# Performance work log

Measured on AMD Instinct MI355X. Metric: run time of the kernel, lower is better.

## Reference

```python
import jax, jax.numpy as jnp
import numpy as np
import math

B, S, D, H = 2, 2048, 2048, 16
DH = D // H  # 128


def _rope(x, cos, sin):
    # x: [b, s, h, dh]; cos/sin: [s, dh//2]
    b, s, h, dh = x.shape
    x2 = x.reshape(b, s, h, dh // 2, 2)
    a, bb = x2[..., 0], x2[..., 1]
    c = cos[None, :, None, :]
    sn = sin[None, :, None, :]
    out = jnp.stack([a * c - bb * sn, a * sn + bb * c], axis=-1)
    return out.reshape(b, s, h, dh)


def setup_inputs() -> dict:
    key = jax.random.key(0)
    ks = jax.random.split(key, 6)
    x = jax.random.normal(ks[0], (B, S, D), dtype=jnp.float32)
    # RoPE frequencies (theta=10000) as cos/sin of shape [S, DH//2]
    inv_freq = 1.0 / (10000.0 ** (np.arange(0, DH, 2, dtype=np.float32) / DH))
    t = np.arange(S, dtype=np.float32)
    ang = jnp.asarray(np.outer(t, inv_freq))  # [S, DH//2]
    freqs_cos = jnp.cos(ang)
    freqs_sin = jnp.sin(ang)
    # causal additive mask [1,1,S,S]
    neg = jnp.finfo(jnp.float32).min
    mask = jnp.where(jnp.tril(jnp.ones((S, S), dtype=bool)), 0.0, neg)[None, None]
    sc = 0.02
    wq = jax.random.normal(ks[1], (D, D), dtype=jnp.float32) * sc
    wk = jax.random.normal(ks[2], (D, D), dtype=jnp.float32) * sc
    wv = jax.random.normal(ks[3], (D, D), dtype=jnp.float32) * sc
    wo = jax.random.normal(ks[4], (D, D), dtype=jnp.float32) * sc
    return {"x": x, "freqs_cos": freqs_cos, "freqs_sin": freqs_sin,
            "mask": mask, "wq": wq, "wk": wk, "wv": wv, "wo": wo}


def reference(x, freqs_cos, freqs_sin, mask, wq, wk, wv, wo):
    b, s, _ = x.shape
    # torch Linear: y = x @ W.T (weights stored [out, in])
    xq = (x @ wq.T).reshape(b, s, H, DH)
    xk = (x @ wk.T).reshape(b, s, H, DH)
    xv = (x @ wv.T).reshape(b, s, H, DH)
    xq = _rope(xq, freqs_cos, freqs_sin)
    xk = _rope(xk, freqs_cos, freqs_sin)
    # [b, h, s, dh]
    q = xq.transpose(0, 2, 1, 3)
    k = xk.transpose(0, 2, 1, 3)
    v = xv.transpose(0, 2, 1, 3)
    scores = jnp.einsum('bhqd,bhkd->bhqk', q, k) / math.sqrt(DH)
    scores = scores + mask
    attn = jax.nn.softmax(scores, axis=-1)  # dropout p=0 (eval)
    out = jnp.einsum('bhqk,bhkd->bhqd', attn, v)
    out = out.transpose(0, 2, 1, 3).reshape(b, s, D)
    return out @ wo.T
```

## Files before the change

kernel.cpp:

```cpp
#include <hip/hip_runtime.h>

#define B_ 2
#define S_ 2048
#define D_ 2048
#define H_ 16
#define DH_ 128

typedef __bf16 bf16_8 __attribute__((ext_vector_type(8)));
typedef __bf16 bf16_4 __attribute__((ext_vector_type(4)));
typedef float f32x4 __attribute__((ext_vector_type(4)));

__device__ __forceinline__ f32x4 mfma16(bf16_8 a, bf16_8 b, f32x4 c) {
  return __builtin_amdgcn_mfma_f32_16x16x32_bf16(a, b, c, 0, 0, 0);
}

__device__ __forceinline__ bf16_8 load8(const float* p) {
  f32x4 a = *(const f32x4*)p;
  f32x4 b = *(const f32x4*)(p + 4);
  bf16_8 r;
  r[0] = (__bf16)a[0]; r[1] = (__bf16)a[1]; r[2] = (__bf16)a[2]; r[3] = (__bf16)a[3];
  r[4] = (__bf16)b[0]; r[5] = (__bf16)b[1]; r[6] = (__bf16)b[2]; r[7] = (__bf16)b[3];
  return r;
}

__device__ __forceinline__ void async16(const __bf16* g, __bf16* l) {
  __builtin_amdgcn_global_load_lds(
      (const __attribute__((address_space(1))) void*)g,
      (__attribute__((address_space(3))) void*)l, 16, 0, 0);
}

__global__ __launch_bounds__(256) void cvt_all(
    const float* __restrict__ x, const float* __restrict__ wq,
    const float* __restrict__ wk, const float* __restrict__ wv,
    const float* __restrict__ wo, __bf16* __restrict__ xb,
    __bf16* __restrict__ wqb, __bf16* __restrict__ wkb,
    __bf16* __restrict__ wvb, __bf16* __restrict__ wob)
{
  const int W8 = (D_ * D_) / 8;
  int i = blockIdx.x * 256 + threadIdx.x;
  if (i < 2 * W8) {
    *(bf16_8*)(xb + (size_t)i * 8) = load8(x + (size_t)i * 8);
  } else {
    int j = i - 2 * W8;
    int sel = j >> 19, off = j & (W8 - 1);
    const float* s = sel == 0 ? wq : sel == 1 ? wk : sel == 2 ? wv : wo;
    __bf16* d = sel == 0 ? wqb : sel == 1 ? wkb : sel == 2 ? wvb : wob;
    *(bf16_8*)(d + (size_t)off * 8) = load8(s + (size_t)off * 8);
  }
}

template <bool WB>
__global__ __launch_bounds__(256) void qkv_gemm(
    const __bf16* __restrict__ A,
    const float* __restrict__ wqf, const float* __restrict__ wkf,
    const float* __restrict__ wvf,
    const __bf16* __restrict__ wqb, const __bf16* __restrict__ wkb,
    const __bf16* __restrict__ wvb,
    const float* __restrict__ fc, const float* __restrict__ fs,
    __bf16* __restrict__ Qo, __bf16* __restrict__ Ko, __bf16* __restrict__ Vo)
{
  __shared__ __bf16 As[128][32];
  __shared__ __bf16 Ws[128][WB ? 32 : 40];
  const int tid = threadIdx.x;
  const int wave = tid >> 6, lane = tid & 63;
  const int quad = lane >> 4, l16 = lane & 15;
  const int m0 = blockIdx.y * 128, n0 = blockIdx.x * 128;
  const int wsel = n0 >> 11, nloc = n0 & 2047;
  const int wm = (wave >> 1) * 64, wn = (wave & 1) * 64;
  const __bf16* agl = A + (size_t)(m0 + wave * 32 + (lane >> 2)) * 2048 + (lane & 3) * 8;
  f32x4 acc[4][4] = {};
  if (WB) {
    const __bf16* Wb = wsel == 0 ? wqb : wsel == 1 ? wkb : wvb;
    const __bf16* wgl = Wb + (size_t)(nloc + wave * 32 + (lane >> 2)) * 2048 + (lane & 3) * 8;
    for (int k0 = 0; k0 < 2048; k0 += 32) {
      __syncthreads();
      async16(agl + k0,             &As[wave * 32][0]);
      async16(agl + 16 * 2048 + k0, &As[wave * 32 + 16][0]);
      async16(wgl + k0,             &Ws[wave * 32][0]);
      async16(wgl + 16 * 2048 + k0, &Ws[wave * 32 + 16][0]);
      __syncthreads();
      bf16_8 af[4], bfr[4];
      for (int i = 0; i < 4; ++i) {
        af[i]  = *(const bf16_8*)&As[wm + i * 16 + l16][quad * 8];
        bfr[i] = *(const bf16_8*)&Ws[wn + i * 16 + l16][quad * 8];
      }
      for (int mi = 0; mi < 4; ++mi)
        for (int ni = 0; ni < 4; ++ni)
          acc[mi][ni] = mfma16(af[mi], bfr[ni], acc[mi][ni]);
    }
  } else {
    const float* W = wsel == 0 ? wqf : wsel == 1 ? wkf : wvf;
    const int srow = tid >> 1, scol = (tid & 1) * 16;
    const float* wg = W + (size_t)(nloc + srow) * 2048 + scol;
    for (int k0 = 0; k0 < 2048; k0 += 32) {
      __syncthreads();
      async16(agl + k0,             &As[wave * 32][0]);
      async16(agl + 16 * 2048 + k0, &As[wave * 32 + 16][0]);
      *(bf16_8*)&Ws[srow][scol]     = load8(wg + k0);
      *(bf16_8*)&Ws[srow][scol + 8] = load8(wg + k0 + 8);
      __syncthreads();
      bf16_8 af[4], bfr[4];
      for (int i = 0; i < 4; ++i) {
        af[i]  = *(const bf16_8*)&As[wm + i * 16 + l16][quad * 8];
        bfr[i] = *(const bf16_8*)&Ws[wn + i * 16 + l16][quad * 8];
      }
      for (int mi = 0; mi < 4; ++mi)
        for (int ni = 0; ni < 4; ++ni)
          acc[mi][ni] = mfma16(af[mi], bfr[ni], acc[mi][ni]);
    }
  }
  if (wsel < 2) {
    const float qscale = wsel == 0 ? 0.08838834764831845f * 1.4426950408889634f
                                   : 1.0f;
    __bf16* O = wsel == 0 ? Qo : Ko;
    for (int mi = 0; mi < 4; ++mi)
      for (int ni = 0; ni < 4; ++ni)
        for (int r = 0; r < 4; ++r) {
          int row = m0 + wm + mi * 16 + quad * 4 + r;
          int col = nloc + wn + ni * 16 + l16;
          float self = acc[mi][ni][r];
          float oth = __shfl_xor(self, 1);
          int s = row & (S_ - 1);
          int dh = col & (DH_ - 1);
          float c = fc[s * (DH_ / 2) + (dh >> 1)];
          float sn = fs[s * (DH_ / 2) + (dh >> 1)];
          float o = (dh & 1) ? (oth * sn + self * c) : (self * c - oth * sn);
          O[(size_t)row * 2048 + col] = (__bf16)(o * qscale);
        }
  } else {
    for (int mi = 0; mi < 4; ++mi)
      for (int ni = 0; ni < 4; ++ni) {
        int col = nloc + wn + ni * 16 + l16;
        int row0 = m0 + wm + mi * 16 + quad * 4;
        int b = row0 >> 11, s = row0 & (S_ - 1);
        int h = col >> 7, dh = col & (DH_ - 1);
        bf16_4 pk;
        for (int r = 0; r < 4; ++r) pk[r] = (__bf16)acc[mi][ni][r];
        *(bf16_4*)(Vo + ((size_t)(b * H_ + h) * DH_ + dh) * S_ + s) = pk;
      }
  }
}

template <bool WB>
__global__ __launch_bounds__(256) void out_gemm(
    const __bf16* __restrict__ A, const float* __restrict__ Wf,
    const __bf16* __restrict__ Wb, float* __restrict__ C)
{
  __shared__ __bf16 As[128][32];
  __shared__ __bf16 Ws[128][WB ? 32 : 40];
  const int tid = threadIdx.x;
  const int wave = tid >> 6, lane = tid & 63;
  const int quad = lane >> 4, l16 = lane & 15;
  const int m0 = blockIdx.y * 128, n0 = blockIdx.x * 128;
  const int wm = (wave >> 1) * 64, wn = (wave & 1) * 64;
  const __bf16* agl = A + (size_t)(m0 + wave * 32 + (lane >> 2)) * 2048 + (lane & 3) * 8;
  f32x4 acc[4][4] = {};
  if (WB) {
    const __bf16* wgl = Wb + (size_t)(n0 + wave * 32 + (lane >> 2)) * 2048 + (lane & 3) * 8;
    for (int k0 = 0; k0 < 2048; k0 += 32) {
      __syncthreads();
      async16(agl + k0,             &As[wave * 32][0]);
      async16(agl + 16 * 2048 + k0, &As[wave * 32 + 16][0]);
      async16(wgl + k0,             &Ws[wave * 32][0]);
      async16(wgl + 16 * 2048 + k0, &Ws[wave * 32 + 16][0]);
      __syncthreads();
      bf16_8 af[4], bfr[4];
      for (int i = 0; i < 4; ++i) {
        af[i]  = *(const bf16_8*)&As[wm + i * 16 + l16][quad * 8];
        bfr[i] = *(const bf16_8*)&Ws[wn + i * 16 + l16][quad * 8];
      }
      for (int mi = 0; mi < 4; ++mi)
        for (int ni = 0; ni < 4; ++ni)
          acc[mi][ni] = mfma16(af[mi], bfr[ni], acc[mi][ni]);
    }
  } else {
    const int srow = tid >> 1, scol = (tid & 1) * 16;
    const float* wg = Wf + (size_t)(n0 + srow) * 2048 + scol;
    for (int k0 = 0; k0 < 2048; k0 += 32) {
      __syncthreads();
      async16(agl + k0,             &As[wave * 32][0]);
      async16(agl + 16 * 2048 + k0, &As[wave * 32 + 16][0]);
      *(bf16_8*)&Ws[srow][scol]     = load8(wg + k0);
      *(bf16_8*)&Ws[srow][scol + 8] = load8(wg + k0 + 8);
      __syncthreads();
      bf16_8 af[4], bfr[4];
      for (int i = 0; i < 4; ++i) {
        af[i]  = *(const bf16_8*)&As[wm + i * 16 + l16][quad * 8];
        bfr[i] = *(const bf16_8*)&Ws[wn + i * 16 + l16][quad * 8];
      }
      for (int mi = 0; mi < 4; ++mi)
        for (int ni = 0; ni < 4; ++ni)
          acc[mi][ni] = mfma16(af[mi], bfr[ni], acc[mi][ni]);
    }
  }
  for (int mi = 0; mi < 4; ++mi)
    for (int ni = 0; ni < 4; ++ni)
      for (int r = 0; r < 4; ++r) {
        int row = m0 + wm + mi * 16 + quad * 4 + r;
        int col = n0 + wn + ni * 16 + l16;
        C[(size_t)row * 2048 + col] = acc[mi][ni][r];
      }
}

__global__ __launch_bounds__(256) void attn_kernel(
    const __bf16* __restrict__ Q, const __bf16* __restrict__ K,
    const __bf16* __restrict__ Vt_g, __bf16* __restrict__ O)
{
  __shared__ __bf16 Ks[64 * 128];
  __shared__ __bf16 Vt[128 * 64];
  __shared__ __bf16 Ps[4][32][72];
  const int tid = threadIdx.x;
  const int wave = tid >> 6, lane = tid & 63;
  const int quad = lane >> 4, l16 = lane & 15;
  const int qt = gridDim.x - 1 - blockIdx.x;
  const int bh = blockIdx.y;
  const size_t base = (size_t)(bh >> 4) * S_ * D_ + (size_t)(bh & 15) * DH_;
  const size_t vtb = (size_t)bh * DH_ * S_;
  const int q0 = qt * 128;
  const int wmin = q0 + wave * 32;

  bf16_8 qf[2][4];
  for (int qs = 0; qs < 2; ++qs) {
    int qrow = wmin + qs * 16 + l16;
    for (int kk = 0; kk < 4; ++kk)
      qf[qs][kk] = *(const bf16_8*)(Q + base + (size_t)qrow * D_ + kk * 32 + quad * 8);
  }

  const int krs = wave * 4 + (lane >> 4);
  const __bf16* kgl = K + base + (size_t)krs * D_ + ((lane & 15) ^ krs) * 8;
  const int vrs = wave * 8 + (lane >> 3);
  const __bf16* vgl = Vt_g + vtb + (size_t)vrs * S_ + ((lane & 7) ^ (lane >> 3)) * 8;

  f32x4 oacc[2][8] = {};
  float lsum[2][4] = {};
  const int nt = 2 * qt + 2;

  for (int kt = 0; kt < nt; ++kt) {
    __syncthreads();
    for (int p = 0; p < 4; ++p)
      async16(kgl + (size_t)(kt * 64 + p * 16) * D_, Ks + (p * 16 + wave * 4) * 128);
    for (int p = 0; p < 4; ++p)
      async16(vgl + (size_t)(p * 32) * S_ + kt * 64, Vt + (p * 32 + wave * 8) * 64);
    __syncthreads();
    if (kt * 64 > wmin + 31) continue;

    const bool diag = (kt * 64 + 63 > wmin);
    for (int n = 0; n < 4; ++n) {
      f32x4 s0 = {}, s1 = {};
#pragma unroll
      for (int kk = 0; kk < 4; ++kk) {
        bf16_8 kf = *(const bf16_8*)&Ks[(n * 16 + l16) * 128 + (((kk * 4 + quad) ^ l16) * 8)];
        s0 = mfma16(qf[0][kk], kf, s0);
        s1 = mfma16(qf[1][kk], kf, s1);
      }
#pragma unroll
      for (int qs = 0; qs < 2; ++qs) {
        f32x4 sv = qs ? s1 : s0;
        for (int r = 0; r < 4; ++r) {
          float v = sv[r];
          if (diag) {
            int qr = wmin + qs * 16 + quad * 4 + r;
            if (kt * 64 + n * 16 + l16 > qr) v = -INFINITY;
          }
          float p = exp2f(v);
          lsum[qs][r] += p;
          Ps[wave][qs * 16 + quad * 4 + r][n * 16 + l16] = (__bf16)p;
        }
      }
    }
    bf16_8 pf0[2], pf1[2];
    for (int qs = 0; qs < 2; ++qs) {
      pf0[qs] = *(const bf16_8*)&Ps[wave][qs * 16 + l16][quad * 8];
      pf1[qs] = *(const bf16_8*)&Ps[wave][qs * 16 + l16][32 + quad * 8];
    }
#pragma unroll
    for (int nc = 0; nc < 8; ++nc) {
      bf16_8 vf0 = *(const bf16_8*)&Vt[(nc * 16 + l16) * 64 + ((quad ^ (l16 & 7)) * 8)];
      bf16_8 vf1 = *(const bf16_8*)&Vt[(nc * 16 + l16) * 64 + (((quad + 4) ^ (l16 & 7)) * 8)];
      oacc[0][nc] = mfma16(pf0[0], vf0, oacc[0][nc]);
      oacc[0][nc] = mfma16(pf1[0], vf1, oacc[0][nc]);
      oacc[1][nc] = mfma16(pf0[1], vf0, oacc[1][nc]);
      oacc[1][nc] = mfma16(pf1[1], vf1, oacc[1][nc]);
    }
  }

  for (int qs = 0; qs < 2; ++qs)
    for (int r = 0; r < 4; ++r) {
      float l = lsum[qs][r];
      l += __shfl_xor(l, 1);
      l += __shfl_xor(l, 2);
      l += __shfl_xor(l, 4);
      l += __shfl_xor(l, 8);
      float rinv = 1.f / l;
      int qr = wmin + qs * 16 + quad * 4 + r;
      for (int nc = 0; nc < 8; ++nc)
        O[base + (size_t)qr * D_ + nc * 16 + l16] = (__bf16)(oacc[qs][nc][r] * rinv);
    }
}

extern "C" void kernel_launch(void* const* d_in, const int* in_sizes, int n_in,
                              void* d_out, int out_size, void* d_ws, size_t ws_size,
                              hipStream_t stream)
{
  const float* x    = (const float*)d_in[0];
  const float* fcos = (const float*)d_in[1];
  const float* fsin = (const float*)d_in[2];
  const float* wq   = (const float*)d_in[4];
  const float* wk   = (const float*)d_in[5];
  const float* wv   = (const float*)d_in[6];
  const float* wo   = (const float*)d_in[7];
  float* out = (float*)d_out;

  const size_t T = (size_t)B_ * S_ * D_;
  const size_t W = (size_t)D_ * D_;
  __bf16* xb  = (__bf16*)d_ws;
  __bf16* qw  = xb + T;
  __bf16* kw  = qw + T;
  __bf16* vt  = kw + T;
  __bf16* wqb = vt + T;
  __bf16* wkb = wqb + W;
  __bf16* wvb = wkb + W;
  __bf16* wob = wvb + W;
  __bf16* ow  = xb;

  const bool wb = ws_size >= (4 * T + 4 * W) * sizeof(__bf16);
  const int W8 = (int)(W / 8);
  cvt_all<<<(wb ? 6 : 2) * W8 / 256, 256, 0, stream>>>(
      x, wq, wk, wv, wo, xb, wqb, wkb, wvb, wob);
  if (wb)
    qkv_gemm<true><<<dim3(48, 32), 256, 0, stream>>>(
        xb, nullptr, nullptr, nullptr, wqb, wkb, wvb, fcos, fsin, qw, kw, vt);
  else
    qkv_gemm<false><<<dim3(48, 32), 256, 0, stream>>>(
        xb, wq, wk, wv, nullptr, nullptr, nullptr, fcos, fsin, qw, kw, vt);
  attn_kernel<<<dim3(S_ / 128, B_ * H_), 256, 0, stream>>>(qw, kw, vt, ow);
  if (wb)
    out_gemm<true><<<dim3(16, 32), 256, 0, stream>>>(ow, nullptr, wob, out);
  else
    out_gemm<false><<<dim3(16, 32), 256, 0, stream>>>(ow, wo, nullptr, out);
}
```

Baseline: 453.8 us.

## Double-buffer attention K/V tiles, widen GEMM K-step, remap attention grid

The GEMM kernels now stage 64-wide K slices per iteration instead of 32, which halves the number of barrier pairs and packs more MFMAs between synchronisations. The attention kernel switches to 32-key tiles in double-buffered LDS so the next K/V tile is prefetched while the current one is computed. It also moves to a 1-D grid with a remapped ordering of heads and query tiles, intended to balance causal work and improve cache locality. The cost is more LDS per GEMM block, which may lower occupancy, and smaller attention tiles that need more loop iterations.

Result: no change. 458.7 us (+1.1%).

```diff
diff --git a/kernel.cpp b/kernel.cpp
--- a/kernel.cpp
+++ b/kernel.cpp
@@ -59,54 +59,63 @@
     const float* __restrict__ fc, const float* __restrict__ fs,
     __bf16* __restrict__ Qo, __bf16* __restrict__ Ko, __bf16* __restrict__ Vo)
 {
-  __shared__ __bf16 As[128][32];
-  __shared__ __bf16 Ws[128][WB ? 32 : 40];
+  __shared__ __bf16 As[128][64];
+  __shared__ __bf16 Ws[128][64];
   const int tid = threadIdx.x;
   const int wave = tid >> 6, lane = tid & 63;
   const int quad = lane >> 4, l16 = lane & 15;
   const int m0 = blockIdx.y * 128, n0 = blockIdx.x * 128;
   const int wsel = n0 >> 11, nloc = n0 & 2047;
   const int wm = (wave >> 1) * 64, wn = (wave & 1) * 64;
-  const __bf16* agl = A + (size_t)(m0 + wave * 32 + (lane >> 2)) * 2048 + (lane & 3) * 8;
+  const __bf16* agl = A + (size_t)(m0 + wave * 32 + (lane >> 3)) * 2048 + (lane & 7) * 8;
   f32x4 acc[4][4] = {};
   if (WB) {
     const __bf16* Wb = wsel == 0 ? wqb : wsel == 1 ? wkb : wvb;
-    const __bf16* wgl = Wb + (size_t)(nloc + wave * 32 + (lane >> 2)) * 2048 + (lane & 3) * 8;
-    for (int k0 = 0; k0 < 2048; k0 += 32) {
-      __syncthreads();
-      async16(agl + k0,             &As[wave * 32][0]);
-      async16(agl + 16 * 2048 + k0, &As[wave * 32 + 16][0]);
-      async16(wgl + k0,             &Ws[wave * 32][0]);
-      async16(wgl + 16 * 2048 + k0, &Ws[wave * 32 + 16][0]);
-      __syncthreads();
-      bf16_8 af[4], bfr[4];
-      for (int i = 0; i < 4; ++i) {
-        af[i]  = *(const bf16_8*)&As[wm + i * 16 + l16][quad * 8];
-        bfr[i] = *(const bf16_8*)&Ws[wn + i * 16 + l16][quad * 8];
-      }
-      for (int mi = 0; mi < 4; ++mi)
-        for (int ni = 0; ni < 4; ++ni)
-          acc[mi][ni] = mfma16(af[mi], bfr[ni], acc[mi][ni]);
+    const __bf16* wgl = Wb + (size_t)(nloc + wave * 32 + (lane >> 3)) * 2048 + (lane & 7) * 8;
+    for (int k0 = 0; k0 < 2048; k0 += 64) {
+      __syncthreads();
+#pragma unroll
+      for (int p = 0; p < 4; ++p) {
+        async16(agl + (size_t)(p * 8) * 2048 + k0, &As[wave * 32 + p * 8][0]);
+        async16(wgl + (size_t)(p * 8) * 2048 + k0, &Ws[wave * 32 + p * 8][0]);
+      }
+      __syncthreads();
+#pragma unroll
+      for (int h = 0; h < 2; ++h) {
+        bf16_8 af[4], bfr[4];
+        for (int i = 0; i < 4; ++i) {
+          af[i]  = *(const bf16_8*)&As[wm + i * 16 + l16][h * 32 + quad * 8];
+          bfr[i] = *(const bf16_8*)&Ws[wn + i * 16 + l16][h * 32 + quad * 8];
+        }
+        for (int mi = 0; mi < 4; ++mi)
+          for (int ni = 0; ni < 4; ++ni)
+            acc[mi][ni] = mfma16(af[mi], bfr[ni], acc[mi][ni]);
+      }
     }
   } else {
     const float* W = wsel == 0 ? wqf : wsel == 1 ? wkf : wvf;
-    const int srow = tid >> 1, scol = (tid & 1) * 16;
-    const float* wg = W + (size_t)(nloc + srow) * 2048 + scol;
-    for (int k0 = 0; k0 < 2048; k0 += 32) {
-      __syncthreads();
-      async16(agl + k0,             &As[wave * 32][0]);
-      async16(agl + 16 * 2048 + k0, &As[wave * 32 + 16][0]);
-      *(bf16_8*)&Ws[srow][scol]     = load8(wg + k0);
-      *(bf16_8*)&Ws[srow][scol + 8] = load8(wg + k0 + 8);
-      __syncthreads();
-      bf16_8 af[4], bfr[4];
-      for (int i = 0; i < 4; ++i) {
-        af[i]  = *(const bf16_8*)&As[wm + i * 16 + l16][quad * 8];
-        bfr[i] = *(const bf16_8*)&Ws[wn + i * 16 + l16][quad * 8];
-      }
-      for (int mi = 0; mi < 4; ++mi)
-        for (int ni = 0; ni < 4; ++ni)
-          acc[mi][ni] = mfma16(af[mi], bfr[ni], acc[mi][ni]);
+    const int srow = tid >> 1, scol0 = (tid & 1) * 32;
+    const float* wg = W + (size_t)(nloc + srow) * 2048 + scol0;
+    for (int k0 = 0; k0 < 2048; k0 += 64) {
+      __syncthreads();
+#pragma unroll
+      for (int p = 0; p < 4; ++p)
+        async16(agl + (size_t)(p * 8) * 2048 + k0, &As[wave * 32 + p * 8][0]);
+#pragma unroll
+      for (int j = 0; j < 4; ++j)
+        *(bf16_8*)&Ws[srow][scol0 + j * 8] = load8(wg + k0 + j * 8);
+      __syncthreads();
+#pragma unroll
+      for (int h = 0; h < 2; ++h) {
+        bf16_8 af[4], bfr[4];
+        for (int i = 0; i < 4; ++i) {
+          af[i]  = *(const bf16_8*)&As[wm + i * 16 + l16][h * 32 + quad * 8];
+          bfr[i] = *(const bf16_8*)&Ws[wn + i * 16 + l16][h * 32 + quad * 8];
+        }
+        for (int mi = 0; mi < 4; ++mi)
+          for (int ni = 0; ni < 4; ++ni)
+            acc[mi][ni] = mfma16(af[mi], bfr[ni], acc[mi][ni]);
+      }
     }
   }
   if (wsel < 2) {
@@ -146,51 +155,60 @@
     const __bf16* __restrict__ A, const float* __restrict__ Wf,
     const __bf16* __restrict__ Wb, float* __restrict__ C)
 {
-  __shared__ __bf16 As[128][32];
-  __shared__ __bf16 Ws[128][WB ? 32 : 40];
+  __shared__ __bf16 As[128][64];
+  __shared__ __bf16 Ws[128][64];
   const int tid = threadIdx.x;
   const int wave = tid >> 6, lane = tid & 63;
   const int quad = lane >> 4, l16 = lane & 15;
   const int m0 = blockIdx.y * 128, n0 = blockIdx.x * 128;
   const int wm = (wave >> 1) * 64, wn = (wave & 1) * 64;
-  const __bf16* agl = A + (size_t)(m0 + wave * 32 + (lane >> 2)) * 2048 + (lane & 3) * 8;
+  const __bf16* agl = A + (size_t)(m0 + wave * 32 + (lane >> 3)) * 2048 + (lane & 7) * 8;
   f32x4 acc[4][4] = {};
   if (WB) {
-    const __bf16* wgl = Wb + (size_t)(n0 + wave * 32 + (lane >> 2)) * 2048 + (lane & 3) * 8;
-    for (int k0 = 0; k0 < 2048; k0 += 32) {
-      __syncthreads();
-      async16(agl + k0,             &As[wave * 32][0]);
-      async16(agl + 16 * 2048 + k0, &As[wave * 32 + 16][0]);
-      async16(wgl + k0,             &Ws[wave * 32][0]);
-      async16(wgl + 16 * 2048 + k0, &Ws[wave * 32 + 16][0]);
-      __syncthreads();
-      bf16_8 af[4], bfr[4];
-      for (int i = 0; i < 4; ++i) {
-        af[i]  = *(const bf16_8*)&As[wm + i * 16 + l16][quad * 8];
-        bfr[i] = *(const bf16_8*)&Ws[wn + i * 16 + l16][quad * 8];
-      }
-      for (int mi = 0; mi < 4; ++mi)
-        for (int ni = 0; ni < 4; ++ni)
-          acc[mi][ni] = mfma16(af[mi], bfr[ni], acc[mi][ni]);
+    const __bf16* wgl = Wb + (size_t)(n0 + wave * 32 + (lane >> 3)) * 2048 + (lane & 7) * 8;
+    for (int k0 = 0; k0 < 2048; k0 += 64) {
+      __syncthreads();
+#pragma unroll
+      for (int p = 0; p < 4; ++p) {
+        async16(agl + (size_t)(p * 8) * 2048 + k0, &As[wave * 32 + p * 8][0]);
+        async16(wgl + (size_t)(p * 8) * 2048 + k0, &Ws[wave * 32 + p * 8][0]);
+      }
+      __syncthreads();
+#pragma unroll
+      for (int h = 0; h < 2; ++h) {
+        bf16_8 af[4], bfr[4];
+        for (int i = 0; i < 4; ++i) {
+          af[i]  = *(const bf16_8*)&As[wm + i * 16 + l16][h * 32 + quad * 8];
+          bfr[i] = *(const bf16_8*)&Ws[wn + i * 16 + l16][h * 32 + quad * 8];
+        }
+        for (int mi = 0; mi < 4; ++mi)
+          for (int ni = 0; ni < 4; ++ni)
+            acc[mi][ni] = mfma16(af[mi], bfr[ni], acc[mi][ni]);
+      }
     }
   } else {
-    const int srow = tid >> 1, scol = (tid & 1) * 16;
-    const float* wg = Wf + (size_t)(n0 + srow) * 2048 + scol;
-    for (int k0 = 0; k0 < 2048; k0 += 32) {
-      __syncthreads();
-      async16(agl + k0,             &As[wave * 32][0]);
-      async16(agl + 16 * 2048 + k0, &As[wave * 32 + 16][0]);
-      *(bf16_8*)&Ws[srow][scol]     = load8(wg + k0);
-      *(bf16_8*)&Ws[srow][scol + 8] = load8(wg + k0 + 8);
-      __syncthreads();
-      bf16_8 af[4], bfr[4];
-      for (int i = 0; i < 4; ++i) {
-        af[i]  = *(const bf16_8*)&As[wm + i * 16 + l16][quad * 8];
-        bfr[i] = *(const bf16_8*)&Ws[wn + i * 16 + l16][quad * 8];
-      }
-      for (int mi = 0; mi < 4; ++mi)
-        for (int ni = 0; ni < 4; ++ni)
-          acc[mi][ni] = mfma16(af[mi], bfr[ni], acc[mi][ni]);
+    const int srow = tid >> 1, scol0 = (tid & 1) * 32;
+    const float* wg = Wf + (size_t)(n0 + srow) * 2048 + scol0;
+    for (int k0 = 0; k0 < 2048; k0 += 64) {
+      __syncthreads();
+#pragma unroll
+      for (int p = 0; p < 4; ++p)
+        async16(agl + (size_t)(p * 8) * 2048 + k0, &As[wave * 32 + p * 8][0]);
+#pragma unroll
+      for (int j = 0; j < 4; ++j)
+        *(bf16_8*)&Ws[srow][scol0 + j * 8] = load8(wg + k0 + j * 8);
+      __syncthreads();
+#pragma unroll
+      for (int h = 0; h < 2; ++h) {
+        bf16_8 af[4], bfr[4];
+        for (int i = 0; i < 4; ++i) {
+          af[i]  = *(const bf16_8*)&As[wm + i * 16 + l16][h * 32 + quad * 8];
+          bfr[i] = *(const bf16_8*)&Ws[wn + i * 16 + l16][h * 32 + quad * 8];
+        }
+        for (int mi = 0; mi < 4; ++mi)
+          for (int ni = 0; ni < 4; ++ni)
+            acc[mi][ni] = mfma16(af[mi], bfr[ni], acc[mi][ni]);
+      }
     }
   }
   for (int mi = 0; mi < 4; ++mi)
@@ -206,14 +224,15 @@
     const __bf16* __restrict__ Q, const __bf16* __restrict__ K,
     const __bf16* __restrict__ Vt_g, __bf16* __restrict__ O)
 {
-  __shared__ __bf16 Ks[64 * 128];
-  __shared__ __bf16 Vt[128 * 64];
-  __shared__ __bf16 Ps[4][32][72];
+  __shared__ __bf16 Ks[2][32 * 128];
+  __shared__ __bf16 Vt[2][128 * 32];
+  __shared__ __bf16 Ps[4][32][40];
   const int tid = threadIdx.x;
   const int wave = tid >> 6, lane = tid & 63;
   const int quad = lane >> 4, l16 = lane & 15;
-  const int qt = gridDim.x - 1 - blockIdx.x;
-  const int bh = blockIdx.y;
+  const int bid = blockIdx.x;
+  const int bh = (bid & 7) * 4 + (bid >> 7);
+  const int qt = 15 - ((bid >> 3) & 15);
   const size_t base = (size_t)(bh >> 4) * S_ * D_ + (size_t)(bh & 15) * DH_;
   const size_t vtb = (size_t)bh * DH_ * S_;
   const int q0 = qt * 128;
@@ -228,59 +247,66 @@
 
   const int krs = wave * 4 + (lane >> 4);
   const __bf16* kgl = K + base + (size_t)krs * D_ + ((lane & 15) ^ krs) * 8;
-  const int vrs = wave * 8 + (lane >> 3);
-  const __bf16* vgl = Vt_g + vtb + (size_t)vrs * S_ + ((lane & 7) ^ (lane >> 3)) * 8;
+  const int vrs = (lane >> 2) & 3;
+  const __bf16* vgl = Vt_g + vtb + (size_t)(wave * 16 + (lane >> 2)) * S_ +
+                      ((lane & 3) ^ vrs) * 8;
 
   f32x4 oacc[2][8] = {};
   float lsum[2][4] = {};
-  const int nt = 2 * qt + 2;
-
-  for (int kt = 0; kt < nt; ++kt) {
+  const int ktmax = (q0 >> 5) + 3;
+
+  for (int p = 0; p < 2; ++p)
+    async16(kgl + (size_t)(p * 16) * D_, &Ks[0][(p * 16 + wave * 4) * 128]);
+  for (int p = 0; p < 2; ++p)
+    async16(vgl + (size_t)(p * 64) * S_, &Vt[0][(p * 64 + wave * 16) * 32]);
+
+  for (int kt = 0; kt <= ktmax; ++kt) {
+    const int cur = kt & 1;
     __syncthreads();
-    for (int p = 0; p < 4; ++p)
-      async16(kgl + (size_t)(kt * 64 + p * 16) * D_, Ks + (p * 16 + wave * 4) * 128);
-    for (int p = 0; p < 4; ++p)
-      async16(vgl + (size_t)(p * 32) * S_ + kt * 64, Vt + (p * 32 + wave * 8) * 64);
-    __syncthreads();
-    if (kt * 64 > wmin + 31) continue;
-
-    const bool diag = (kt * 64 + 63 > wmin);
-    for (int n = 0; n < 4; ++n) {
+    if (kt < ktmax) {
+      const int nk = (kt + 1) * 32;
+      for (int p = 0; p < 2; ++p)
+        async16(kgl + (size_t)(nk + p * 16) * D_, &Ks[cur ^ 1][(p * 16 + wave * 4) * 128]);
+      for (int p = 0; p < 2; ++p)
+        async16(vgl + (size_t)(p * 64) * S_ + nk, &Vt[cur ^ 1][(p * 64 + wave * 16) * 32]);
+    }
+    if (kt * 32 > wmin + 31) continue;
+
+    const bool diag = (kt * 32 + 31 > wmin);
+    float sc[2][2][4];
+#pragma unroll
+    for (int n = 0; n < 2; ++n) {
       f32x4 s0 = {}, s1 = {};
 #pragma unroll
       for (int kk = 0; kk < 4; ++kk) {
-        bf16_8 kf = *(const bf16_8*)&Ks[(n * 16 + l16) * 128 + (((kk * 4 + quad) ^ l16) * 8)];
+        bf16_8 kf = *(const bf16_8*)&Ks[cur][(n * 16 + l16) * 128 +
+                                            (((kk * 4 + quad) ^ l16) * 8)];
         s0 = mfma16(qf[0][kk], kf, s0);
         s1 = mfma16(qf[1][kk], kf, s1);
       }
-#pragma unroll
-      for (int qs = 0; qs < 2; ++qs) {
-        f32x4 sv = qs ? s1 : s0;
-        for (int r = 0; r < 4; ++r) {
-          float v = sv[r];
+      for (int r = 0; r < 4; ++r) { sc[0][n][r] = s0[r]; sc[1][n][r] = s1[r]; }
+    }
+#pragma unroll
+    for (int qs = 0; qs < 2; ++qs)
+      for (int r = 0; r < 4; ++r)
+        for (int n = 0; n < 2; ++n) {
+          float v = sc[qs][n][r];
           if (diag) {
             int qr = wmin + qs * 16 + quad * 4 + r;
-            if (kt * 64 + n * 16 + l16 > qr) v = -INFINITY;
+            if (kt * 32 + n * 16 + l16 > qr) v = -INFINITY;
           }
           float p = exp2f(v);
           lsum[qs][r] += p;
           Ps[wave][qs * 16 + quad * 4 + r][n * 16 + l16] = (__bf16)p;
         }
-      }
-    }
-    bf16_8 pf0[2], pf1[2];
-    for (int qs = 0; qs < 2; ++qs) {
-      pf0[qs] = *(const bf16_8*)&Ps[wave][qs * 16 + l16][quad * 8];
-      pf1[qs] = *(const bf16_8*)&Ps[wave][qs * 16 + l16][32 + quad * 8];
-    }
+    bf16_8 pf0 = *(const bf16_8*)&Ps[wave][l16][quad * 8];
+    bf16_8 pf1 = *(const bf16_8*)&Ps[wave][16 + l16][quad * 8];
 #pragma unroll
     for (int nc = 0; nc < 8; ++nc) {
-      bf16_8 vf0 = *(const bf16_8*)&Vt[(nc * 16 + l16) * 64 + ((quad ^ (l16 & 7)) * 8)];
-      bf16_8 vf1 = *(const bf16_8*)&Vt[(nc * 16 + l16) * 64 + (((quad + 4) ^ (l16 & 7)) * 8)];
-      oacc[0][nc] = mfma16(pf0[0], vf0, oacc[0][nc]);
-      oacc[0][nc] = mfma16(pf1[0], vf1, oacc[0][nc]);
-      oacc[1][nc] = mfma16(pf0[1], vf0, oacc[1][nc]);
-      oacc[1][nc] = mfma16(pf1[1], vf1, oacc[1][nc]);
+      bf16_8 vf = *(const bf16_8*)&Vt[cur][(nc * 16 + l16) * 32 +
+                                           ((quad ^ (l16 & 3)) * 8)];
+      oacc[0][nc] = mfma16(pf0, vf, oacc[0][nc]);
+      oacc[1][nc] = mfma16(pf1, vf, oacc[1][nc]);
     }
   }
 
@@ -333,7 +359,7 @@
   else
     qkv_gemm<false><<<dim3(48, 32), 256, 0, stream>>>(
         xb, wq, wk, wv, nullptr, nullptr, nullptr, fcos, fsin, qw, kw, vt);
-  attn_kernel<<<dim3(S_ / 128, B_ * H_), 256, 0, stream>>>(qw, kw, vt, ow);
+  attn_kernel<<<dim3((S_ / 128) * B_ * H_), 256, 0, stream>>>(qw, kw, vt, ow);
   if (wb)
     out_gemm<true><<<dim3(16, 32), 256, 0, stream>>>(ow, nullptr, wob, out);
   else
```
